# Optimization experiments

Hardware: AMD Instinct MI355X
Metric: run time of the kernel (lower is better)

## Reference

```python
import jax, jax.numpy as jnp
import numpy as np
import math

DIM = 1024
HEADS = 16
HEAD_DIM = DIM // HEADS
ROT = min(HEAD_DIM, 32)  # rotary_dim
B, S = 2, 1024


def setup_inputs() -> dict:
    key = jax.random.key(0)
    ks = jax.random.split(key, 32)
    lin = lambda k: jax.random.normal(k, (DIM, DIM), jnp.float32) * 0.02
    bias = lambda k: jax.random.normal(k, (DIM,), jnp.float32) * 0.01
    inp = {
        'real': jax.random.normal(ks[0], (B, S, DIM), jnp.float32),
        'imag': jax.random.normal(ks[1], (B, S, DIM), jnp.float32),
        'Wq_r': lin(ks[2]), 'bq_r': bias(ks[3]),
        'Wk_r': lin(ks[4]), 'bk_r': bias(ks[5]),
        'Wv_r': lin(ks[6]), 'bv_r': bias(ks[7]),
        'Wq_i': lin(ks[8]), 'bq_i': bias(ks[9]),
        'Wk_i': lin(ks[10]), 'bk_i': bias(ks[11]),
        'Wv_i': lin(ks[12]), 'bv_i': bias(ks[13]),
        'Wo_r': lin(ks[14]), 'bo_r': bias(ks[15]),
        'Wo_i': lin(ks[16]), 'bo_i': bias(ks[17]),
        'phase_shifts': jax.random.normal(ks[18], (HEADS, HEAD_DIM), jnp.float32) * 0.02,
        'ent': jnp.eye(HEADS, dtype=jnp.float32) + jax.random.normal(ks[19], (HEADS, HEADS), jnp.float32) * 0.01,
        'rot_freqs': (10000.0 ** (-jnp.arange(0, ROT, 2, dtype=jnp.float32) / ROT)),
        'strength': jnp.ones((1,), jnp.float32),
        'temp': jnp.ones((1,), jnp.float32),
    }
    return inp


def _fwd(real, imag, Wq_r, bq_r, Wk_r, bk_r, Wv_r, bv_r,
         Wq_i, bq_i, Wk_i, bk_i, Wv_i, bv_i,
         Wo_r, bo_r, Wo_i, bo_i,
         phase_shifts, ent, rot_freqs, strength, temp):
    b, s, _ = real.shape
    to_heads = lambda t: t.reshape(b, s, HEADS, HEAD_DIM).transpose(0, 2, 1, 3)  # bhsd
    lin = lambda x, W, bb: x @ W + bb

    q_r = to_heads(lin(real, Wq_r, bq_r))
    k_r = to_heads(lin(real, Wk_r, bk_r))
    v_r = to_heads(lin(real, Wv_r, bv_r))
    q_i = to_heads(lin(imag, Wq_i, bq_i))
    k_i = to_heads(lin(imag, Wk_i, bk_i))
    v_i = to_heads(lin(imag, Wv_i, bv_i))

    # rotary on first ROT dims (pairwise rotation)
    pos = jnp.arange(s, dtype=jnp.float32)
    emb = pos[:, None] * rot_freqs[None, :]           # [S, ROT/2]
    cos = jnp.cos(emb)[None, None]                    # [1,1,S,ROT/2]
    sin = jnp.sin(emb)[None, None]

    def rope(t):
        tr = t[..., :ROT].reshape(b, HEADS, s, ROT // 2, 2)
        r0 = tr[..., 0] * cos - tr[..., 1] * sin
        r1 = tr[..., 1] * cos + tr[..., 0] * sin
        rr = jnp.stack([r0, r1], axis=-1).reshape(b, HEADS, s, ROT)
        return jnp.concatenate([rr, t[..., ROT:]], axis=-1)

    q_r, k_r = rope(q_r), rope(k_r)
    q_i, k_i = rope(q_i), rope(k_i)

    # entanglement mixing across heads
    mix = lambda t: jnp.einsum('bhsd,hx->bxsd', t, ent)
    q_r, q_i, k_r, k_i = mix(q_r), mix(q_i), mix(k_r), mix(k_i)

    # per-head phase shift (complex rotation)
    pc = jnp.cos(phase_shifts)[None, :, None, :]      # [1,H,1,D]
    ps = jnp.sin(phase_shifts)[None, :, None, :]
    q_r, q_i = q_r * pc - q_i * ps, q_r * ps + q_i * pc
    k_r, k_i = k_r * pc - k_i * ps, k_r * ps + k_i * pc

    scale = 1.0 / math.sqrt(HEAD_DIM)
    attn_r = (jnp.einsum('bhqd,bhkd->bhqk', q_r, k_r) + jnp.einsum('bhqd,bhkd->bhqk', q_i, k_i)) * scale
    attn_i = (jnp.einsum('bhqd,bhkd->bhqk', q_i, k_r) - jnp.einsum('bhqd,bhkd->bhqk', q_r, k_i)) * scale
    attn_mag = jnp.sqrt(attn_r ** 2 + attn_i ** 2 + 1e-6)

    causal = jnp.triu(jnp.ones((s, s), dtype=bool), k=1)[None, None]
    attn_mag = jnp.where(causal, -jnp.inf, attn_mag)

    t = jnp.maximum(temp, 0.01)
    g = jax.nn.sigmoid(strength)
    attn = jax.nn.softmax(attn_mag * g / t, axis=-1)

    out_r = jnp.einsum('bhqk,bhkd->bhqd', attn, v_r).transpose(0, 2, 1, 3).reshape(b, s, DIM)
    out_i = jnp.einsum('bhqk,bhkd->bhqd', attn, v_i).transpose(0, 2, 1, 3).reshape(b, s, DIM)
    return lin(out_r, Wo_r, bo_r), lin(out_i, Wo_i, bo_i)


def reference(real, imag, Wq_r, bq_r, Wk_r, bk_r, Wv_r, bv_r,
              Wq_i, bq_i, Wk_i, bk_i, Wv_i, bv_i,
              Wo_r, bo_r, Wo_i, bo_i,
              phase_shifts, ent, rot_freqs, strength, temp):
    return _fwd(real, imag, Wq_r, bq_r, Wk_r, bk_r, Wv_r, bv_r,
                Wq_i, bq_i, Wk_i, bk_i, Wv_i, bv_i,
                Wo_r, bo_r, Wo_i, bo_i,
                phase_shifts, ent, rot_freqs, strength, temp)
```

## Files before the change

kernel.cpp:

```cpp
#include <hip/hip_runtime.h>
#include <stdint.h>

typedef unsigned short u16;
typedef __bf16 bf16x8 __attribute__((ext_vector_type(8)));
typedef float f32x4 __attribute__((ext_vector_type(4)));
typedef unsigned int u32x4 __attribute__((ext_vector_type(4)));

__device__ __forceinline__ u16 f2bf(float f) {
  uint32_t u = __float_as_uint(f);
  u += 0x7FFFu + ((u >> 16) & 1u);
  return (u16)(u >> 16);
}
__device__ __forceinline__ float bf2f(u16 h) {
  return __uint_as_float(((uint32_t)h) << 16);
}
__device__ __forceinline__ float fsqrt(float x) {
  float r; asm("v_sqrt_f32 %0, %1" : "=v"(r) : "v"(x)); return r;
}
__device__ __forceinline__ void gld16(const void* g, void* lds) {
  __builtin_amdgcn_global_load_lds(
      (const __attribute__((address_space(1))) uint32_t*)g,
      (__attribute__((address_space(3))) uint32_t*)lds, 16, 0, 0);
}
__device__ __forceinline__ f32x4 mfma16(u32x4 a, u32x4 b, f32x4 c) {
  return __builtin_amdgcn_mfma_f32_16x16x32_bf16(
      __builtin_bit_cast(bf16x8, a), __builtin_bit_cast(bf16x8, b), c, 0, 0, 0);
}

__global__ __launch_bounds__(256) void tables_kernel(const float* __restrict__ rotf,
                                                     const float* __restrict__ phase,
                                                     float* __restrict__ T) {
  int id = blockIdx.x * 256 + threadIdx.x;
  if (id < 16384) {
    int s = id >> 4, jj = id & 15;
    float sn, cs;
    sincosf((float)s * rotf[jj], &sn, &cs);
    T[id] = cs;
    T[16384 + id] = sn;
  } else if (id < 16384 + 1024) {
    int p = id - 16384;
    float sn, cs;
    sincosf(phase[p], &sn, &cs);
    T[32768 + p] = cs;
    T[33792 + p] = sn;
  }
}

__global__ __launch_bounds__(256) void convx_kernel(const float* __restrict__ real,
                                                    const float* __restrict__ imag,
                                                    u16* __restrict__ Xr,
                                                    u16* __restrict__ Xi) {
  int u = blockIdx.x * 256 + threadIdx.x;
  int a = u >> 18;
  int r = u & 262143;
  int m = r >> 7, slot = r & 127;
  const float* src = (a ? imag : real) + (size_t)m * 1024 + slot * 8;
  int slot2 = (slot & ~7) | ((slot ^ m) & 7);
  u16* dst = (a ? Xi : Xr) + (size_t)m * 1024 + slot2 * 8;
  f32x4 v0 = *(const f32x4*)(src);
  f32x4 v1 = *(const f32x4*)(src + 4);
  union { u16 h[8]; u32x4 v; } o;
#pragma unroll
  for (int e = 0; e < 4; ++e) { o.h[e] = f2bf(v0[e]); o.h[4 + e] = f2bf(v1[e]); }
  *(u32x4*)dst = o.v;
}

__global__ __launch_bounds__(256) void convw_kernel(
    const float* __restrict__ w0, const float* __restrict__ w1,
    const float* __restrict__ w2, const float* __restrict__ w3,
    const float* __restrict__ w4, const float* __restrict__ w5,
    const float* __restrict__ w6, const float* __restrict__ w7,
    u16* __restrict__ WtAll) {
  __shared__ float Lt[64][65];
  int z = blockIdx.z;
  const float* W = (z == 0) ? w0 : (z == 1) ? w1 : (z == 2) ? w2 : (z == 3) ? w3
                 : (z == 4) ? w4 : (z == 5) ? w5 : (z == 6) ? w6 : w7;
  u16* Wt = WtAll + (size_t)z * (1024 * 1024);
  int tid = threadIdx.x;
  int n0 = blockIdx.x * 64, k0 = blockIdx.y * 64;
#pragma unroll
  for (int it = 0; it < 4; ++it) {
    int idx = it * 256 + tid;
    int kr = idx >> 4, nc = (idx & 15) * 4;
    f32x4 v = *(const f32x4*)(W + (size_t)(k0 + kr) * 1024 + n0 + nc);
#pragma unroll
    for (int e = 0; e < 4; ++e) Lt[kr][nc + e] = v[e];
  }
  __syncthreads();
#pragma unroll
  for (int it = 0; it < 2; ++it) {
    int idx = it * 256 + tid;
    int nr = idx >> 3, sl = idx & 7;
    union { u16 h[8]; u32x4 v; } o;
#pragma unroll
    for (int e = 0; e < 8; ++e) o.h[e] = f2bf(Lt[sl * 8 + e][nr]);
    int sl2 = sl ^ (nr & 7);
    *(u32x4*)(Wt + (size_t)(n0 + nr) * 1024 + k0 + sl2 * 8) = o.v;
  }
}

__device__ __forceinline__ void gemm128(const u16* __restrict__ A, const u16* __restrict__ W,
                                        const float* __restrict__ bias,
                                        u16* __restrict__ outB, float* __restrict__ outF) {
  __shared__ __align__(16) u16 As[128 * 64];
  __shared__ __align__(16) u16 Bs[128 * 64];
  int tid = threadIdx.x, l = tid & 63, w = tid >> 6;
  int lr = l & 15, lh = l >> 4;
  int m0 = blockIdx.y * 128, n0 = blockIdx.x * 128;
  int wr = w >> 1, wc = w & 1;
  f32x4 acc[4][4];
#pragma unroll
  for (int mi = 0; mi < 4; ++mi)
#pragma unroll
    for (int ni = 0; ni < 4; ++ni) acc[mi][ni] = f32x4{0.f, 0.f, 0.f, 0.f};

  for (int kt = 0; kt < 16; ++kt) {
#pragma unroll
    for (int c = 0; c < 4; ++c) {
      int chunk = c * 4 + w;
      int i = chunk * 64 + l;
      int row = i >> 3, off = i & 7;
      gld16(A + (size_t)(m0 + row) * 1024 + kt * 64 + off * 8, (char*)As + chunk * 1024);
      gld16(W + (size_t)(n0 + row) * 1024 + kt * 64 + off * 8, (char*)Bs + chunk * 1024);
    }
    __syncthreads();
#pragma unroll
    for (int kk = 0; kk < 2; ++kk) {
      u32x4 af[4], bf[4];
#pragma unroll
      for (int mi = 0; mi < 4; ++mi) {
        int row = wr * 64 + mi * 16 + lr;
        af[mi] = *(const u32x4*)((const char*)As + row * 128 +
                                 ((kk * 64 + lh * 16) ^ ((row & 7) << 4)));
      }
#pragma unroll
      for (int ni = 0; ni < 4; ++ni) {
        int row = wc * 64 + ni * 16 + lr;
        bf[ni] = *(const u32x4*)((const char*)Bs + row * 128 +
                                 ((kk * 64 + lh * 16) ^ ((row & 7) << 4)));
      }
#pragma unroll
      for (int mi = 0; mi < 4; ++mi)
#pragma unroll
        for (int ni = 0; ni < 4; ++ni)
          acc[mi][ni] = mfma16(af[mi], bf[ni], acc[mi][ni]);
    }
    __syncthreads();
  }
#pragma unroll
  for (int ni = 0; ni < 4; ++ni) {
    int col = n0 + wc * 64 + ni * 16 + lr;
    float bv = bias[col];
#pragma unroll
    for (int mi = 0; mi < 4; ++mi)
#pragma unroll
      for (int rr = 0; rr < 4; ++rr) {
        int row = m0 + wr * 64 + mi * 16 + 4 * lh + rr;
        float v = acc[mi][ni][rr] + bv;
        if (outF) outF[(size_t)row * 1024 + col] = v;
        else      outB[(size_t)row * 1024 + col] = f2bf(v);
      }
  }
}

__global__ __launch_bounds__(256) void gemm_proj_kernel(
    const u16* __restrict__ Xr, const u16* __restrict__ Xi, const u16* __restrict__ Wt,
    const float* b0, const float* b1, const float* b2,
    const float* b3, const float* b4, const float* b5,
    u16* __restrict__ qkv) {
  int z = blockIdx.z;
  const u16* A = (z < 3) ? Xr : Xi;
  const u16* W = Wt + (size_t)z * (1024 * 1024);
  const float* bias = (z == 0) ? b0 : (z == 1) ? b1 : (z == 2) ? b2
                    : (z == 3) ? b3 : (z == 4) ? b4 : b5;
  u16* out = qkv + (size_t)z * (2048 * 1024);
  gemm128(A, W, bias, out, nullptr);
}

__global__ __launch_bounds__(256) void gemm_out_kernel(
    const u16* __restrict__ O, const u16* __restrict__ Wt2,
    const float* br, const float* bi, float* __restrict__ dout) {
  int z = blockIdx.z;
  gemm128(O + (size_t)z * (2048 * 1024), Wt2 + (size_t)z * (1024 * 1024),
          z ? bi : br, nullptr, dout + (size_t)z * (2048 * 1024));
}

__global__ __launch_bounds__(256) void transform_kernel(
    const u16* __restrict__ qkv, const float* __restrict__ ent,
    const float* __restrict__ T,
    u16* __restrict__ Qr, u16* __restrict__ Qi, u16* __restrict__ Kr,
    u16* __restrict__ Ki, u16* __restrict__ Vr, u16* __restrict__ Vi) {
  __shared__ float Lqr[16][65], Lqi[16][65], Lkr[16][65], Lki[16][65];
  __shared__ float sent[256];
  int tid = threadIdx.x;
  int bs = blockIdx.x;
  int b = bs >> 10, s = bs & 1023;
  sent[tid] = ent[tid];
  const u16* qr_raw = qkv;
  const u16* kr_raw = qkv + (size_t)1 * 2048 * 1024;
  const u16* vr_raw = qkv + (size_t)2 * 2048 * 1024;
  const u16* qi_raw = qkv + (size_t)3 * 2048 * 1024;
  const u16* ki_raw = qkv + (size_t)4 * 2048 * 1024;
  const u16* vi_raw = qkv + (size_t)5 * 2048 * 1024;
  size_t rowoff = (size_t)bs * 1024;
#pragma unroll
  for (int it = 0; it < 2; ++it) {
    int u = it * 256 + tid;
    int hh = u >> 5, j = u & 31;
    int base = hh * 64 + 2 * j;
    uint32_t aqr = *(const uint32_t*)(qr_raw + rowoff + base);
    uint32_t aqi = *(const uint32_t*)(qi_raw + rowoff + base);
    uint32_t akr = *(const uint32_t*)(kr_raw + rowoff + base);
    uint32_t aki = *(const uint32_t*)(ki_raw + rowoff + base);
    float qr0 = bf2f((u16)aqr), qr1 = bf2f((u16)(aqr >> 16));
    float qi0 = bf2f((u16)aqi), qi1 = bf2f((u16)(aqi >> 16));
    float kr0 = bf2f((u16)akr), kr1 = bf2f((u16)(akr >> 16));
    float ki0 = bf2f((u16)aki), ki1 = bf2f((u16)(aki >> 16));
    if (j < 16) {
      float cs = T[s * 16 + j];
      float sn = T[16384 + s * 16 + j];
      float t0;
      t0 = qr0; qr0 = t0 * cs - qr1 * sn; qr1 = qr1 * cs + t0 * sn;
      t0 = qi0; qi0 = t0 * cs - qi1 * sn; qi1 = qi1 * cs + t0 * sn;
      t0 = kr0; kr0 = t0 * cs - kr1 * sn; kr1 = kr1 * cs + t0 * sn;
      t0 = ki0; ki0 = t0 * cs - ki1 * sn; ki1 = ki1 * cs + t0 * sn;
    }
    int d0 = 2 * j;
    Lqr[hh][d0] = qr0; Lqr[hh][d0 + 1] = qr1;
    Lqi[hh][d0] = qi0; Lqi[hh][d0 + 1] = qi1;
    Lkr[hh][d0] = kr0; Lkr[hh][d0 + 1] = kr1;
    Lki[hh][d0] = ki0; Lki[hh][d0 + 1] = ki1;
  }
  __syncthreads();
#pragma unroll
  for (int it = 0; it < 4; ++it) {
    int u = it * 256 + tid;
    int x = u >> 6, d = u & 63;
    float mqr = 0.f, mqi = 0.f, mkr = 0.f, mki = 0.f;
#pragma unroll
    for (int hh = 0; hh < 16; ++hh) {
      float e = sent[hh * 16 + x];
      mqr += Lqr[hh][d] * e; mqi += Lqi[hh][d] * e;
      mkr += Lkr[hh][d] * e; mki += Lki[hh][d] * e;
    }
    float pc_ = T[32768 + x * 64 + d];
    float ps_ = T[33792 + x * 64 + d];
    float oqr = (mqr * pc_ - mqi * ps_) * 0.125f;
    float oqi = (mqr * ps_ + mqi * pc_) * 0.125f;
    float okr = mkr * pc_ - mki * ps_;
    float oki = mkr * ps_ + mki * pc_;
    size_t obase = ((size_t)(b * 16 + x) * 1024 + s) * 64;
    Qr[obase + d] = f2bf(oqr);
    Qi[obase + d] = f2bf(oqi);
    int dsw = (d & 7) | ((((d >> 3) ^ s) & 7) << 3);
    Kr[obase + dsw] = f2bf(okr);
    Ki[obase + dsw] = f2bf(oki);
  }
  {
    int u = tid;
    int comp = u >> 7, hh = (u >> 3) & 15, sl = u & 7;
    const u16* src = comp ? vi_raw : vr_raw;
    u16* dst = comp ? Vi : Vr;
    u32x4 vv = *(const u32x4*)(src + rowoff + hh * 64 + sl * 8);
    *(u32x4*)(dst + ((size_t)(b * 16 + hh) * 1024 + s) * 64 + sl * 8) = vv;
  }
}

__global__ __launch_bounds__(256) void transv_kernel(const u16* __restrict__ Vr,
                                                     const u16* __restrict__ Vi,
                                                     u16* __restrict__ VTr,
                                                     u16* __restrict__ VTi) {
  int bid = blockIdx.x;
  int comp = bid >> 9, bh = (bid >> 4) & 31, t = bid & 15;
  const u16* src = (comp ? Vi : Vr) + ((size_t)bh * 1024 + t * 64) * 64;
  u16* dst = (comp ? VTi : VTr) + (size_t)bh * 65536;
  __shared__ __align__(16) u16 Lt[64][72];
  int tid = threadIdx.x;
#pragma unroll
  for (int it = 0; it < 2; ++it) {
    int i = it * 256 + tid;
    int r = i >> 3, sl = i & 7;
    *(u32x4*)(&Lt[r][sl * 8]) = *(const u32x4*)(src + r * 64 + sl * 8);
  }
  __syncthreads();
#pragma unroll
  for (int it = 0; it < 2; ++it) {
    int i = it * 256 + tid;
    int d = i >> 3, sl = i & 7;
    union { u16 h[8]; u32x4 v; } o;
#pragma unroll
    for (int e = 0; e < 8; ++e) o.h[e] = Lt[sl * 8 + e][d];
    int sl2 = sl ^ (d & 7);
    *(u32x4*)(dst + (size_t)d * 1024 + t * 64 + sl2 * 8) = o.v;
  }
}

__global__ __launch_bounds__(256) void attn_kernel(
    const u16* __restrict__ Qr, const u16* __restrict__ Qi,
    const u16* __restrict__ Kr, const u16* __restrict__ Ki,
    const u16* __restrict__ VTr, const u16* __restrict__ VTi,
    const float* __restrict__ strength, const float* __restrict__ temp,
    u16* __restrict__ por0, u16* __restrict__ por1,
    u16* __restrict__ por2, u16* __restrict__ por3,
    u16* __restrict__ poi0, u16* __restrict__ poi1,
    u16* __restrict__ poi2, u16* __restrict__ poi3,
    float* __restrict__ Pm, float* __restrict__ Pl) {
  __shared__ __align__(16) u16 smem[20480];
  char* sb = (char*)smem;
  const int PO = 32768;
  int tid = threadIdx.x, l = tid & 63, w = tid >> 6;
  int lr = l & 15, lh = l >> 4;
  int id = blockIdx.x;
  int x = id & 7, j = id >> 3;
  int bh = x + 8 * (j & 3);
  int cc = j >> 2;
  int qb, sp;
  if (cc < 16)      { qb = 15 - (cc >> 2); sp = cc & 3; }
  else if (cc < 28) { int r = cc - 16; int q3 = r / 3; qb = 11 - q3; sp = r - 3 * q3; }
  else if (cc < 36) { int r = cc - 28; qb = 7 - (r >> 1); sp = r & 1; }
  else              { qb = 39 - cc; sp = 0; }
  int q0 = qb * 64;
  int t0 = sp * 4, t1 = min(qb + 1, t0 + 4);
  int b = bh >> 4; (void)b;
  u16* POr = (sp == 0) ? por0 : (sp == 1) ? por1 : (sp == 2) ? por2 : por3;
  u16* POi = (sp == 0) ? poi0 : (sp == 1) ? poi1 : (sp == 2) ? poi2 : poi3;

  float g = 1.f / (1.f + __expf(-strength[0]));
  float tt = fmaxf(temp[0], 0.01f);
  float gt = g / tt;

  size_t qbase = ((size_t)bh * 1024 + q0 + w * 16 + lr) * 64 + lh * 8;
  u32x4 qrF[2], qiF[2], nqrF[2];
#pragma unroll
  for (int kk = 0; kk < 2; ++kk) {
    qrF[kk] = *(const u32x4*)(Qr + qbase + kk * 32);
    qiF[kk] = *(const u32x4*)(Qi + qbase + kk * 32);
    nqrF[kk] = qrF[kk] ^ 0x80008000u;
  }
  f32x4 o_r[4], o_i[4];
#pragma unroll
  for (int n = 0; n < 4; ++n) { o_r[n] = f32x4{0,0,0,0}; o_i[n] = f32x4{0,0,0,0}; }
  float m_run[4], l_run[4];
#pragma unroll
  for (int rr = 0; rr < 4; ++rr) { m_run[rr] = -__builtin_inff(); l_run[rr] = 0.f; }

  const u16* gK = ((w == 1) ? Ki : Kr) + ((size_t)bh * 1024 + t0 * 64) * 64 + l * 8;
  char* ldK = sb + (w == 1 ? 8192 : 0);
  const u16* gV = ((w == 3) ? VTi : VTr) + (size_t)bh * 65536 + t0 * 64 +
                  (l >> 3) * 1024 + (l & 7) * 8;
  char* ldV = sb + (w == 3 ? 24576 : 16384);

  for (int t = t0; t < t1; ++t) {
    if (w < 2) {
#pragma unroll
      for (int c = 0; c < 8; ++c) gld16(gK + c * 512, ldK + c * 1024);
      gK += 4096;
    } else {
#pragma unroll
      for (int c = 0; c < 8; ++c) gld16(gV + c * 8192, ldV + c * 1024);
      gV += 64;
    }
    __syncthreads();

    f32x4 sr[4], si[4];
#pragma unroll
    for (int n = 0; n < 4; ++n) { sr[n] = f32x4{0,0,0,0}; si[n] = f32x4{0,0,0,0}; }
#pragma unroll
    for (int kk = 0; kk < 2; ++kk) {
#pragma unroll
      for (int n = 0; n < 4; ++n) {
        int kv = n * 16 + lr;
        int xoff = (kk * 64 + lh * 16) ^ ((kv & 7) << 4);
        u32x4 fkr = *(const u32x4*)(sb + kv * 128 + xoff);
        u32x4 fki = *(const u32x4*)(sb + 8192 + kv * 128 + xoff);
        sr[n] = mfma16(qrF[kk], fkr, sr[n]);
        sr[n] = mfma16(qiF[kk], fki, sr[n]);
        si[n] = mfma16(qiF[kk], fkr, si[n]);
        si[n] = mfma16(nqrF[kk], fki, si[n]);
      }
    }

    float pl[4][4], pm[4];
#pragma unroll
    for (int rr = 0; rr < 4; ++rr) pm[rr] = -__builtin_inff();
    bool diag = (t == qb);
#pragma unroll
    for (int n = 0; n < 4; ++n)
#pragma unroll
      for (int rr = 0; rr < 4; ++rr) {
        float a = sr[n][rr], ci = si[n][rr];
        float mag = fsqrt(a * a + ci * ci + 1e-6f) * gt;
        if (diag) {
          if (n * 16 + lr > w * 16 + 4 * lh + rr) mag = -__builtin_inff();
        }
        pl[n][rr] = mag;
        pm[rr] = fmaxf(pm[rr], mag);
      }
#pragma unroll
    for (int mk = 1; mk <= 8; mk <<= 1)
#pragma unroll
      for (int rr = 0; rr < 4; ++rr)
        pm[rr] = fmaxf(pm[rr], __shfl_xor(pm[rr], mk));

    bool defer = true;
#pragma unroll
    for (int rr = 0; rr < 4; ++rr) defer = defer && (pm[rr] - m_run[rr] <= 8.f);
    bool noresc = __all(defer ? 1 : 0);
    float fr[4];
    if (!noresc) {
#pragma unroll
      for (int rr = 0; rr < 4; ++rr) {
        float mnew = fmaxf(m_run[rr], pm[rr]);
        fr[rr] = __expf(m_run[rr] - mnew);
        m_run[rr] = mnew;
      }
    }
    float rs[4];
#pragma unroll
    for (int rr = 0; rr < 4; ++rr) rs[rr] = 0.f;
#pragma unroll
    for (int n = 0; n < 4; ++n)
#pragma unroll
      for (int rr = 0; rr < 4; ++rr) {
        float p = __expf(pl[n][rr] - m_run[rr]);
        pl[n][rr] = p;
        rs[rr] += p;
      }
#pragma unroll
    for (int mk = 1; mk <= 8; mk <<= 1)
#pragma unroll
      for (int rr = 0; rr < 4; ++rr)
        rs[rr] += __shfl_xor(rs[rr], mk);
    if (!noresc) {
#pragma unroll
      for (int rr = 0; rr < 4; ++rr) l_run[rr] = l_run[rr] * fr[rr] + rs[rr];
#pragma unroll
      for (int n = 0; n < 4; ++n)
#pragma unroll
        for (int rr = 0; rr < 4; ++rr) { o_r[n][rr] *= fr[rr]; o_i[n][rr] *= fr[rr]; }
    } else {
#pragma unroll
      for (int rr = 0; rr < 4; ++rr) l_run[rr] += rs[rr];
    }

    char* pw = sb + PO + w * 2048;
#pragma unroll
    for (int n = 0; n < 4; ++n)
#pragma unroll
      for (int rr = 0; rr < 4; ++rr) {
        int row = 4 * lh + rr, col = n * 16 + lr;
        int by = row * 128 + ((col & 7) * 2) + ((((col >> 3) ^ row) & 7) << 4);
        *(u16*)(pw + by) = f2bf(pl[n][rr]);
      }
    u32x4 pf[2];
#pragma unroll
    for (int kk = 0; kk < 2; ++kk)
      pf[kk] = *(const u32x4*)(pw + lr * 128 + ((kk * 64 + lh * 16) ^ ((lr & 7) << 4)));
#pragma unroll
    for (int kk = 0; kk < 2; ++kk)
#pragma unroll
      for (int n = 0; n < 4; ++n) {
        int dl = n * 16 + lr;
        int xoff = (kk * 64 + lh * 16) ^ ((dl & 7) << 4);
        u32x4 fvr = *(const u32x4*)(sb + 16384 + dl * 128 + xoff);
        u32x4 fvi = *(const u32x4*)(sb + 24576 + dl * 128 + xoff);
        o_r[n] = mfma16(pf[kk], fvr, o_r[n]);
        o_i[n] = mfma16(pf[kk], fvi, o_i[n]);
      }
    __syncthreads();
  }

  size_t pbase = ((size_t)bh * 1024 + q0 + w * 16 + 4 * lh) * 64;
#pragma unroll
  for (int n = 0; n < 4; ++n)
#pragma unroll
    for (int rr = 0; rr < 4; ++rr) {
      POr[pbase + rr * 64 + n * 16 + lr] = f2bf(o_r[n][rr]);
      POi[pbase + rr * 64 + n * 16 + lr] = f2bf(o_i[n][rr]);
    }
  if (lr == 0) {
    size_t mbase = (size_t)sp * 32768 + (size_t)bh * 1024 + q0 + w * 16 + 4 * lh;
#pragma unroll
    for (int rr = 0; rr < 4; ++rr) {
      Pm[mbase + rr] = m_run[rr];
      Pl[mbase + rr] = l_run[rr];
    }
  }
}

__global__ __launch_bounds__(256) void combine_kernel(
    const u16* __restrict__ por0, const u16* __restrict__ por1,
    const u16* __restrict__ por2, const u16* __restrict__ por3,
    const u16* __restrict__ poi0, const u16* __restrict__ poi1,
    const u16* __restrict__ poi2, const u16* __restrict__ poi3,
    const float* __restrict__ Pm, const float* __restrict__ Pl,
    u16* __restrict__ Or, u16* __restrict__ Oi) {
  int bid = blockIdx.x;
  int bh = bid >> 4, rg = bid & 15;
  int b = bh >> 4, h = bh & 15;
  int ns = (rg >> 2) + 1;
  int tid = threadIdx.x;
  int row = tid >> 2, q = tid & 3;
  int s = rg * 64 + row;
  size_t ro = (size_t)bh * 1024 + s;
  const u16* PR[4] = {por0, por1, por2, por3};
  const u16* PI[4] = {poi0, poi1, poi2, poi3};
  float msp[4], lsp[4], csw[4];
  float M = -__builtin_inff();
#pragma unroll
  for (int sp = 0; sp < 4; ++sp) {
    if (sp < ns) {
      msp[sp] = Pm[ro + (size_t)sp * 32768];
      lsp[sp] = Pl[ro + (size_t)sp * 32768];
      M = fmaxf(M, msp[sp]);
    }
  }
  float lt = 0.f;
#pragma unroll
  for (int sp = 0; sp < 4; ++sp) {
    if (sp < ns) { csw[sp] = __expf(msp[sp] - M); lt += lsp[sp] * csw[sp]; }
    else csw[sp] = 0.f;
  }
  float inv = 1.f / lt;
#pragma unroll
  for (int sp = 0; sp < 4; ++sp) csw[sp] *= inv;
  size_t obase = ro * 64;
#pragma unroll
  for (int g = 0; g < 2; ++g) {
    int d = q * 16 + g * 8;
    float accr[8], acci[8];
#pragma unroll
    for (int e = 0; e < 8; ++e) { accr[e] = 0.f; acci[e] = 0.f; }
#pragma unroll
    for (int sp = 0; sp < 4; ++sp) {
      if (sp < ns) {
        union { u16 h[8]; u32x4 v; } ar, ai;
        ar.v = *(const u32x4*)(PR[sp] + obase + d);
        ai.v = *(const u32x4*)(PI[sp] + obase + d);
#pragma unroll
        for (int e = 0; e < 8; ++e) {
          accr[e] += csw[sp] * bf2f(ar.h[e]);
          acci[e] += csw[sp] * bf2f(ai.h[e]);
        }
      }
    }
    union { u16 h[8]; u32x4 v; } outr, outi;
#pragma unroll
    for (int e = 0; e < 8; ++e) { outr.h[e] = f2bf(accr[e]); outi.h[e] = f2bf(acci[e]); }
    int slot2 = (d >> 3) ^ (s & 7);
    size_t oo = ((size_t)b * 1024 + s) * 1024 + h * 64 + slot2 * 8;
    *(u32x4*)(Or + oo) = outr.v;
    *(u32x4*)(Oi + oo) = outi.v;
  }
}

extern "C" void kernel_launch(void* const* d_in, const int* in_sizes, int n_in,
                              void* d_out, int out_size, void* d_ws, size_t ws_size,
                              hipStream_t stream) {
  (void)in_sizes; (void)n_in; (void)out_size; (void)ws_size;
  const float* real = (const float*)d_in[0];
  const float* imag = (const float*)d_in[1];
  const float* bq_r = (const float*)d_in[3];
  const float* bk_r = (const float*)d_in[5];
  const float* bv_r = (const float*)d_in[7];
  const float* bq_i = (const float*)d_in[9];
  const float* bk_i = (const float*)d_in[11];
  const float* bv_i = (const float*)d_in[13];
  const float* bo_r = (const float*)d_in[15];
  const float* bo_i = (const float*)d_in[17];
  const float* phase = (const float*)d_in[18];
  const float* ent = (const float*)d_in[19];
  const float* rotf = (const float*)d_in[20];
  const float* strength = (const float*)d_in[21];
  const float* temp = (const float*)d_in[22];

  u16* ws = (u16*)d_ws;
  const size_t M1 = 1024 * 1024, M2 = 2048 * 1024;
  u16* Xr  = ws;
  u16* Xi  = Xr + M2;
  u16* Wt  = Xi + M2;
  u16* qkv = Wt + 8 * M1;
  u16* Qr  = qkv + 6 * M2;
  u16* Qi  = Qr + M2;
  u16* Kr  = Qi + M2;
  u16* Ki  = Kr + M2;
  u16* Vr  = Ki + M2;
  u16* Vi  = Vr + M2;
  u16* VTr = Vi + M2;
  u16* VTi = VTr + M2;
  u16* Or  = VTi + M2;
  u16* Oi  = Or + M2;
  u16* por0 = qkv;
  u16* por1 = qkv + M2;
  u16* por2 = qkv + 2 * M2;
  u16* por3 = qkv + 3 * M2;
  u16* poi0 = qkv + 4 * M2;
  u16* poi1 = qkv + 5 * M2;
  u16* poi2 = Vr;
  u16* poi3 = Vi;
  float* Pm = (float*)Xr;
  float* Pl = Pm + 131072;
  float* TBL = (float*)Oi;

  tables_kernel<<<68, 256, 0, stream>>>(rotf, phase, TBL);
  convx_kernel<<<2048, 256, 0, stream>>>(real, imag, Xr, Xi);
  convw_kernel<<<dim3(16, 16, 8), 256, 0, stream>>>(
      (const float*)d_in[2],  (const float*)d_in[4],  (const float*)d_in[6],
      (const float*)d_in[8],  (const float*)d_in[10], (const float*)d_in[12],
      (const float*)d_in[14], (const float*)d_in[16], Wt);
  gemm_proj_kernel<<<dim3(8, 16, 6), 256, 0, stream>>>(Xr, Xi, Wt, bq_r, bk_r, bv_r,
                                                       bq_i, bk_i, bv_i, qkv);
  transform_kernel<<<2048, 256, 0, stream>>>(qkv, ent, TBL, Qr, Qi, Kr, Ki, Vr, Vi);
  transv_kernel<<<1024, 256, 0, stream>>>(Vr, Vi, VTr, VTi);
  attn_kernel<<<1280, 256, 0, stream>>>(Qr, Qi, Kr, Ki, VTr, VTi, strength, temp,
                                        por0, por1, por2, por3,
                                        poi0, poi1, poi2, poi3, Pm, Pl);
  combine_kernel<<<512, 256, 0, stream>>>(por0, por1, por2, por3,
                                          poi0, poi1, poi2, poi3, Pm, Pl, Or, Oi);
  gemm_out_kernel<<<dim3(8, 16, 2), 256, 0, stream>>>(Or, Wt + 6 * M1, bo_r, bo_i,
                                                      (float*)d_out);
}
```

Before: 157.1 us.

## Double-buffer GEMM LDS tiles and widen attention blocks to 128 query rows

The shared GEMM routine now keeps two LDS buffers for the A and W tiles and prefetches the next K slice while MFMAs run on the current one. Each attention block now covers 128 query rows with 8 waves and 512 threads instead of 64 rows with 4 waves. All 8 waves share each K/V tile load, which halves K/V traffic per query and halves the grid size. The causal mask now uses global row and column indices so it works for two diagonal tiles. The costs are more LDS per block, fewer blocks in flight and coarser split work, and the tail of the GEMM loop may lack a barrier before a buffer is overwritten.

```diff
diff --git a/kernel.cpp b/kernel.cpp
--- a/kernel.cpp
+++ b/kernel.cpp
@@ -102,8 +102,8 @@
 __device__ __forceinline__ void gemm128(const u16* __restrict__ A, const u16* __restrict__ W,
                                         const float* __restrict__ bias,
                                         u16* __restrict__ outB, float* __restrict__ outF) {
-  __shared__ __align__(16) u16 As[128 * 64];
-  __shared__ __align__(16) u16 Bs[128 * 64];
+  __shared__ __align__(16) u16 As[2][128 * 64];
+  __shared__ __align__(16) u16 Bs[2][128 * 64];
   int tid = threadIdx.x, l = tid & 63, w = tid >> 6;
   int lr = l & 15, lh = l >> 4;
   int m0 = blockIdx.y * 128, n0 = blockIdx.x * 128;
@@ -114,29 +114,45 @@
 #pragma unroll
     for (int ni = 0; ni < 4; ++ni) acc[mi][ni] = f32x4{0.f, 0.f, 0.f, 0.f};
 
+  const u16* aA = A + (size_t)(m0 + w * 8 + (l >> 3)) * 1024 + (l & 7) * 8;
+  const u16* aW = W + (size_t)(n0 + w * 8 + (l >> 3)) * 1024 + (l & 7) * 8;
+  int ldoff = w * 1024 + l * 16;
+
+#pragma unroll
+  for (int c = 0; c < 4; ++c) {
+    gld16(aA + c * 32768, (char*)As[0] + ldoff + c * 4096);
+    gld16(aW + c * 32768, (char*)Bs[0] + ldoff + c * 4096);
+  }
+  __syncthreads();
+
   for (int kt = 0; kt < 16; ++kt) {
-#pragma unroll
-    for (int c = 0; c < 4; ++c) {
-      int chunk = c * 4 + w;
-      int i = chunk * 64 + l;
-      int row = i >> 3, off = i & 7;
-      gld16(A + (size_t)(m0 + row) * 1024 + kt * 64 + off * 8, (char*)As + chunk * 1024);
-      gld16(W + (size_t)(n0 + row) * 1024 + kt * 64 + off * 8, (char*)Bs + chunk * 1024);
-    }
-    __syncthreads();
+    int cur = kt & 1;
+    if (kt < 15) {
+      const u16* nA = aA + (kt + 1) * 64;
+      const u16* nW = aW + (kt + 1) * 64;
+      char* dA = (char*)As[cur ^ 1] + ldoff;
+      char* dB = (char*)Bs[cur ^ 1] + ldoff;
+#pragma unroll
+      for (int c = 0; c < 4; ++c) {
+        gld16(nA + c * 32768, dA + c * 4096);
+        gld16(nW + c * 32768, dB + c * 4096);
+      }
+    }
+    const char* cA = (const char*)As[cur];
+    const char* cB = (const char*)Bs[cur];
 #pragma unroll
     for (int kk = 0; kk < 2; ++kk) {
       u32x4 af[4], bf[4];
 #pragma unroll
       for (int mi = 0; mi < 4; ++mi) {
         int row = wr * 64 + mi * 16 + lr;
-        af[mi] = *(const u32x4*)((const char*)As + row * 128 +
+        af[mi] = *(const u32x4*)(cA + row * 128 +
                                  ((kk * 64 + lh * 16) ^ ((row & 7) << 4)));
       }
 #pragma unroll
       for (int ni = 0; ni < 4; ++ni) {
         int row = wc * 64 + ni * 16 + lr;
-        bf[ni] = *(const u32x4*)((const char*)Bs + row * 128 +
+        bf[ni] = *(const u32x4*)(cB + row * 128 +
                                  ((kk * 64 + lh * 16) ^ ((row & 7) << 4)));
       }
 #pragma unroll
@@ -295,7 +311,7 @@
   }
 }
 
-__global__ __launch_bounds__(256) void attn_kernel(
+__global__ __launch_bounds__(512) void attn_kernel(
     const u16* __restrict__ Qr, const u16* __restrict__ Qi,
     const u16* __restrict__ Kr, const u16* __restrict__ Ki,
     const u16* __restrict__ VTr, const u16* __restrict__ VTi,
@@ -305,7 +321,7 @@
     u16* __restrict__ poi0, u16* __restrict__ poi1,
     u16* __restrict__ poi2, u16* __restrict__ poi3,
     float* __restrict__ Pm, float* __restrict__ Pl) {
-  __shared__ __align__(16) u16 smem[20480];
+  __shared__ __align__(16) u16 smem[24576];
   char* sb = (char*)smem;
   const int PO = 32768;
   int tid = threadIdx.x, l = tid & 63, w = tid >> 6;
@@ -314,13 +330,14 @@
   int x = id & 7, j = id >> 3;
   int bh = x + 8 * (j & 3);
   int cc = j >> 2;
-  int qb, sp;
-  if (cc < 16)      { qb = 15 - (cc >> 2); sp = cc & 3; }
-  else if (cc < 28) { int r = cc - 16; int q3 = r / 3; qb = 11 - q3; sp = r - 3 * q3; }
-  else if (cc < 36) { int r = cc - 28; qb = 7 - (r >> 1); sp = r & 1; }
-  else              { qb = 39 - cc; sp = 0; }
-  int q0 = qb * 64;
-  int t0 = sp * 4, t1 = min(qb + 1, t0 + 4);
+  int qbi, sp;
+  if (cc < 8)       { qbi = 7 - (cc >> 2); sp = cc & 3; }
+  else if (cc < 14) { int r = cc - 8; int q3 = r / 3; qbi = 5 - q3; sp = r - 3 * q3; }
+  else if (cc < 18) { int r = cc - 14; qbi = 3 - (r >> 1); sp = r & 1; }
+  else              { qbi = 19 - cc; sp = 0; }
+  int q0 = qbi * 128;
+  int nt = 2 * qbi + 2;
+  int t0 = sp * 4, t1 = min(nt, t0 + 4);
   int b = bh >> 4; (void)b;
   u16* POr = (sp == 0) ? por0 : (sp == 1) ? por1 : (sp == 2) ? por2 : por3;
   u16* POi = (sp == 0) ? poi0 : (sp == 1) ? poi1 : (sp == 2) ? poi2 : poi3;
@@ -344,21 +361,26 @@
 #pragma unroll
   for (int rr = 0; rr < 4; ++rr) { m_run[rr] = -__builtin_inff(); l_run[rr] = 0.f; }
 
-  const u16* gK = ((w == 1) ? Ki : Kr) + ((size_t)bh * 1024 + t0 * 64) * 64 + l * 8;
-  char* ldK = sb + (w == 1 ? 8192 : 0);
-  const u16* gV = ((w == 3) ? VTi : VTr) + (size_t)bh * 65536 + t0 * 64 +
-                  (l >> 3) * 1024 + (l & 7) * 8;
-  char* ldV = sb + (w == 3 ? 24576 : 16384);
+  int role = w >> 1;
+  int pl = ((w & 1) << 6) | l;
+  const u16* gsrc;
+  if (role < 2) {
+    gsrc = (role ? Ki : Kr) + ((size_t)bh * 1024 + t0 * 64) * 64 + pl * 8;
+  } else {
+    gsrc = (role == 3 ? VTi : VTr) + (size_t)bh * 65536 + t0 * 64 +
+           (pl >> 3) * 1024 + (pl & 7) * 8;
+  }
+  char* ldst = sb + role * 8192 + pl * 16;
 
   for (int t = t0; t < t1; ++t) {
-    if (w < 2) {
-#pragma unroll
-      for (int c = 0; c < 8; ++c) gld16(gK + c * 512, ldK + c * 1024);
-      gK += 4096;
+    if (role < 2) {
+#pragma unroll
+      for (int c = 0; c < 4; ++c) gld16(gsrc + c * 1024, ldst + c * 2048);
+      gsrc += 4096;
     } else {
 #pragma unroll
-      for (int c = 0; c < 8; ++c) gld16(gV + c * 8192, ldV + c * 1024);
-      gV += 64;
+      for (int c = 0; c < 4; ++c) gld16(gsrc + c * 16384, ldst + c * 2048);
+      gsrc += 64;
     }
     __syncthreads();
 
@@ -380,10 +402,10 @@
       }
     }
 
-    float pl[4][4], pm[4];
+    float pl_[4][4], pm[4];
 #pragma unroll
     for (int rr = 0; rr < 4; ++rr) pm[rr] = -__builtin_inff();
-    bool diag = (t == qb);
+    bool diag = (t >= 2 * qbi);
 #pragma unroll
     for (int n = 0; n < 4; ++n)
 #pragma unroll
@@ -391,9 +413,11 @@
         float a = sr[n][rr], ci = si[n][rr];
         float mag = fsqrt(a * a + ci * ci + 1e-6f) * gt;
         if (diag) {
-          if (n * 16 + lr > w * 16 + 4 * lh + rr) mag = -__builtin_inff();
+          int colg = t * 64 + n * 16 + lr;
+          int rowg = q0 + w * 16 + 4 * lh + rr;
+          if (colg > rowg) mag = -__builtin_inff();
         }
-        pl[n][rr] = mag;
+        pl_[n][rr] = mag;
         pm[rr] = fmaxf(pm[rr], mag);
       }
 #pragma unroll
@@ -422,8 +446,8 @@
     for (int n = 0; n < 4; ++n)
 #pragma unroll
       for (int rr = 0; rr < 4; ++rr) {
-        float p = __expf(pl[n][rr] - m_run[rr]);
-        pl[n][rr] = p;
+        float p = __expf(pl_[n][rr] - m_run[rr]);
+        pl_[n][rr] = p;
         rs[rr] += p;
       }
 #pragma unroll
@@ -450,7 +474,7 @@
       for (int rr = 0; rr < 4; ++rr) {
         int row = 4 * lh + rr, col = n * 16 + lr;
         int by = row * 128 + ((col & 7) * 2) + ((((col >> 3) ^ row) & 7) << 4);
-        *(u16*)(pw + by) = f2bf(pl[n][rr]);
+        *(u16*)(pw + by) = f2bf(pl_[n][rr]);
       }
     u32x4 pf[2];
 #pragma unroll
@@ -612,9 +636,9 @@
                                                        bq_i, bk_i, bv_i, qkv);
   transform_kernel<<<2048, 256, 0, stream>>>(qkv, ent, TBL, Qr, Qi, Kr, Ki, Vr, Vi);
   transv_kernel<<<1024, 256, 0, stream>>>(Vr, Vi, VTr, VTi);
-  attn_kernel<<<1280, 256, 0, stream>>>(Qr, Qi, Kr, Ki, VTr, VTi, strength, temp,
-                                        por0, por1, por2, por3,
-                                        poi0, poi1, poi2, poi3, Pm, Pl);
+  attn_kernel<<<640, 512, 0, stream>>>(Qr, Qi, Kr, Ki, VTr, VTi, strength, temp,
+                                       por0, por1, por2, por3,
+                                       poi0, poi1, poi2, poi3, Pm, Pl);
   combine_kernel<<<512, 256, 0, stream>>>(por0, por1, por2, por3,
                                           poi0, poi1, poi2, poi3, Pm, Pl, Or, Oi);
   gemm_out_kernel<<<dim3(8, 16, 2), 256, 0, stream>>>(Or, Wt + 6 * M1, bo_r, bo_i,
```

Result: slower. 164.9 us (+5.0%).

## Double-buffer GEMM LDS tiles to overlap global loads with MFMA compute

Applied to the files above, without the earlier changes.

The 128x128 GEMM tile loop now keeps two LDS buffers for A and W. It issues the direct-to-LDS global loads for the next k-tile before computing on the current one, and uses explicit vmcnt waits with raw s_barrier instead of two __syncthreads per iteration. This aims to hide global memory latency behind MFMA work in the projection GEMMs, at the cost of doubling LDS use (64KB per block), which may reduce occupancy. A variable in the attention kernel is also renamed, with no functional change.

```diff
diff --git a/kernel.cpp b/kernel.cpp
--- a/kernel.cpp
+++ b/kernel.cpp
@@ -102,8 +102,8 @@
 __device__ __forceinline__ void gemm128(const u16* __restrict__ A, const u16* __restrict__ W,
                                         const float* __restrict__ bias,
                                         u16* __restrict__ outB, float* __restrict__ outF) {
-  __shared__ __align__(16) u16 As[128 * 64];
-  __shared__ __align__(16) u16 Bs[128 * 64];
+  __shared__ __align__(16) u16 As[2][128 * 64];
+  __shared__ __align__(16) u16 Bs[2][128 * 64];
   int tid = threadIdx.x, l = tid & 63, w = tid >> 6;
   int lr = l & 15, lh = l >> 4;
   int m0 = blockIdx.y * 128, n0 = blockIdx.x * 128;
@@ -114,29 +114,50 @@
 #pragma unroll
     for (int ni = 0; ni < 4; ++ni) acc[mi][ni] = f32x4{0.f, 0.f, 0.f, 0.f};
 
+  const u16* aA = A + (size_t)(m0 + w * 8 + (l >> 3)) * 1024 + (l & 7) * 8;
+  const u16* aW = W + (size_t)(n0 + w * 8 + (l >> 3)) * 1024 + (l & 7) * 8;
+  int ldoff = w * 1024 + l * 16;
+
+  auto stage = [&](int buf, int kt) {
+    const u16* pA = aA + kt * 64;
+    const u16* pW = aW + kt * 64;
+    char* dA = (char*)As[buf] + ldoff;
+    char* dB = (char*)Bs[buf] + ldoff;
+#pragma unroll
+    for (int c = 0; c < 4; ++c) {
+      gld16(pA + c * 32768, dA + c * 4096);
+      gld16(pW + c * 32768, dB + c * 4096);
+    }
+  };
+
+  stage(0, 0);
+
   for (int kt = 0; kt < 16; ++kt) {
-#pragma unroll
-    for (int c = 0; c < 4; ++c) {
-      int chunk = c * 4 + w;
-      int i = chunk * 64 + l;
-      int row = i >> 3, off = i & 7;
-      gld16(A + (size_t)(m0 + row) * 1024 + kt * 64 + off * 8, (char*)As + chunk * 1024);
-      gld16(W + (size_t)(n0 + row) * 1024 + kt * 64 + off * 8, (char*)Bs + chunk * 1024);
-    }
-    __syncthreads();
+    int cur = kt & 1;
+    if (kt < 15) {
+      stage(cur ^ 1, kt + 1);
+      asm volatile("s_waitcnt vmcnt(8)" ::: "memory");
+    } else {
+      asm volatile("s_waitcnt vmcnt(0)" ::: "memory");
+    }
+    __builtin_amdgcn_sched_barrier(0);
+    asm volatile("s_barrier" ::: "memory");
+
+    const char* cA = (const char*)As[cur];
+    const char* cB = (const char*)Bs[cur];
 #pragma unroll
     for (int kk = 0; kk < 2; ++kk) {
       u32x4 af[4], bf[4];
 #pragma unroll
       for (int mi = 0; mi < 4; ++mi) {
         int row = wr * 64 + mi * 16 + lr;
-        af[mi] = *(const u32x4*)((const char*)As + row * 128 +
+        af[mi] = *(const u32x4*)(cA + row * 128 +
                                  ((kk * 64 + lh * 16) ^ ((row & 7) << 4)));
       }
 #pragma unroll
       for (int ni = 0; ni < 4; ++ni) {
         int row = wc * 64 + ni * 16 + lr;
-        bf[ni] = *(const u32x4*)((const char*)Bs + row * 128 +
+        bf[ni] = *(const u32x4*)(cB + row * 128 +
                                  ((kk * 64 + lh * 16) ^ ((row & 7) << 4)));
       }
 #pragma unroll
@@ -145,7 +166,7 @@
         for (int ni = 0; ni < 4; ++ni)
           acc[mi][ni] = mfma16(af[mi], bf[ni], acc[mi][ni]);
     }
-    __syncthreads();
+    asm volatile("s_barrier" ::: "memory");
   }
 #pragma unroll
   for (int ni = 0; ni < 4; ++ni) {
@@ -380,7 +401,7 @@
       }
     }
 
-    float pl[4][4], pm[4];
+    float pl_[4][4], pm[4];
 #pragma unroll
     for (int rr = 0; rr < 4; ++rr) pm[rr] = -__builtin_inff();
     bool diag = (t == qb);
@@ -393,7 +414,7 @@
         if (diag) {
           if (n * 16 + lr > w * 16 + 4 * lh + rr) mag = -__builtin_inff();
         }
-        pl[n][rr] = mag;
+        pl_[n][rr] = mag;
         pm[rr] = fmaxf(pm[rr], mag);
       }
 #pragma unroll
@@ -422,8 +443,8 @@
     for (int n = 0; n < 4; ++n)
 #pragma unroll
       for (int rr = 0; rr < 4; ++rr) {
-        float p = __expf(pl[n][rr] - m_run[rr]);
-        pl[n][rr] = p;
+        float p = __expf(pl_[n][rr] - m_run[rr]);
+        pl_[n][rr] = p;
         rs[rr] += p;
       }
 #pragma unroll
@@ -450,7 +471,7 @@
       for (int rr = 0; rr < 4; ++rr) {
         int row = 4 * lh + rr, col = n * 16 + lr;
         int by = row * 128 + ((col & 7) * 2) + ((((col >> 3) ^ row) & 7) << 4);
-        *(u16*)(pw + by) = f2bf(pl[n][rr]);
+        *(u16*)(pw + by) = f2bf(pl_[n][rr]);
       }
     u32x4 pf[2];
 #pragma unroll
```

Result: faster. 151.3 us (-3.7%).
